# Performance work log

Measured on AMD Instinct MI355X. Metric: run time of the kernel, lower is better.

## Reference

```python
import jax, jax.numpy as jnp
import numpy as np
from jax import lax

K = 3  # deformable kernel size


def conv2d(x, w, b):
    # x: [B,C,H,W], w: [O,I,kh,kw], 'SAME' padding, stride 1
    out = lax.conv_general_dilated(x, w, (1, 1), 'SAME',
                                   dimension_numbers=('NCHW', 'OIHW', 'NCHW'))
    return out + b[None, :, None, None]


def deform_conv2d(x, dy, dx, mask, dw, db):
    # Deformable conv v2 (torchvision semantics): bilinear sample at
    # p0 + p_k + delta_p_k, zero outside, modulated by sigmoid mask.
    # x:[B,C,H,W]  dy,dx,mask:[B,H,W,K2]  dw:[O,C,K,K]  db:[O]
    B, C, H, W = x.shape
    K2 = K * K
    pad = K // 2
    ky = (jnp.arange(K2) // K).astype(x.dtype) - pad  # kernel row offsets
    kx = (jnp.arange(K2) % K).astype(x.dtype) - pad
    hy = jnp.arange(H, dtype=x.dtype)[:, None, None]
    wx = jnp.arange(W, dtype=x.dtype)[None, :, None]
    py = hy + ky[None, None, :] + dy  # [B,H,W,K2] sample rows
    px = wx + kx[None, None, :] + dx  # [B,H,W,K2] sample cols

    xf = x.reshape(B, C, H * W)
    gat = jax.vmap(lambda xfb, idx: xfb[:, idx])  # -> [B,C,H,W,K2]

    y0 = jnp.floor(py)
    x0 = jnp.floor(px)
    samp = jnp.zeros((B, C, H, W, K2), x.dtype)
    # accumulate the 4 bilinear corners (zero padding outside image)
    for yc, wy in ((y0, y0 + 1.0 - py), (y0 + 1.0, py - y0)):
        for xc, wxx in ((x0, x0 + 1.0 - px), (x0 + 1.0, px - x0)):
            valid = (yc >= 0) & (yc < H) & (xc >= 0) & (xc < W)
            idx = (jnp.clip(yc, 0, H - 1) * W
                   + jnp.clip(xc, 0, W - 1)).astype(jnp.int32)
            wgt = jnp.where(valid, wy * wxx, jnp.zeros((), x.dtype))
            samp = samp + gat(xf, idx) * wgt[:, None]  # [B,C,H,W,K2]

    samp = samp * mask[:, None]  # modulation: [B,1,H,W,K2]
    out = jnp.einsum('bchwk,ock->bohw', samp, dw.reshape(dw.shape[0], C, K2))
    return out + db[None, :, None, None]


def setup_inputs() -> dict:
    key = jax.random.key(0)
    ks = jax.random.split(key, 8)
    B, C, H, W = 8, 64, 128, 128
    K2 = K * K
    x = jax.random.normal(ks[0], (B, C, H, W), jnp.float32)
    # offset conv (3x3) -> 2*K2 channels; small init so offsets are modest
    ow = 0.02 * jax.random.normal(ks[1], (2 * K2, C, 3, 3), jnp.float32)
    ob = jnp.zeros((2 * K2,), jnp.float32)
    # mask conv (3x3) -> K2 channels
    mw = 0.02 * jax.random.normal(ks[2], (K2, C, 3, 3), jnp.float32)
    mb = jnp.zeros((K2,), jnp.float32)
    # deformable conv weights (C->C, KxK)
    dw = (1.0 / np.sqrt(C * K2)) * jax.random.normal(ks[3], (C, C, K, K), jnp.float32)
    db = jnp.zeros((C,), jnp.float32)
    return {'x': x, 'ow': ow, 'ob': ob, 'mw': mw, 'mb': mb, 'dw': dw, 'db': db}


def reference(x, ow, ob, mw, mb, dw, db):
    B, C, H, W = x.shape
    K2 = K * K
    offset = conv2d(x, ow, ob)                    # [B,2K2,H,W]
    mask = jax.nn.sigmoid(conv2d(x, mw, mb))      # [B,K2,H,W]
    off = offset.reshape(B, K2, 2, H, W)
    dy = off[:, :, 0].transpose(0, 2, 3, 1)       # [B,H,W,K2] (torchvision: even=dy)
    dx = off[:, :, 1].transpose(0, 2, 3, 1)
    return deform_conv2d(x, dy, dx, mask.transpose(0, 2, 3, 1), dw, db)
```

## Files before the change

### kernel.cpp

```cpp
#include <hip/hip_runtime.h>

#define BATCH 8
#define CIN   64
#define HW    16384
#define CK    576

typedef __attribute__((ext_vector_type(8))) short bf16x8;
typedef __attribute__((ext_vector_type(4))) float f32x4;
typedef __attribute__((ext_vector_type(2))) float f32x2;
typedef __attribute__((ext_vector_type(4))) unsigned u32x4;

__device__ inline unsigned short f2bf(float f) {
    unsigned int u = __builtin_bit_cast(unsigned int, f);
    u += 0x7FFFu + ((u >> 16) & 1u);
    return (unsigned short)(u >> 16);
}
__device__ inline float bf2f(unsigned short u) {
    return __builtin_bit_cast(float, (unsigned)u << 16);
}
__device__ inline f32x2 upk2(unsigned u) {
    f32x2 r;
    r[0] = __builtin_bit_cast(float, u << 16);
    r[1] = __builtin_bit_cast(float, u & 0xFFFF0000u);
    return r;
}
__device__ inline unsigned pk2bf(f32x2 s) {
    return (unsigned)f2bf(s[0]) | ((unsigned)f2bf(s[1]) << 16);
}


__global__ __launch_bounds__(256) void prep_transpose(
        const float* __restrict__ x, const float* __restrict__ ow,
        const float* __restrict__ mw, const float* __restrict__ dw,
        unsigned short* __restrict__ wpack, unsigned short* __restrict__ wcpack,
        unsigned short* __restrict__ xT) {
    __shared__ unsigned tile[64 * 36];
    int t = threadIdx.x, blk = blockIdx.x;
    int b = blk & 7, r2 = blk >> 3;
    int h = r2 >> 1, hf = r2 & 1;
    int px0 = hf << 6;
    {
        const float* __restrict__ xb = x + (b * CIN) * HW + (h << 7) + px0;
#pragma unroll
        for (int r = 0; r < 2; r++) {
            int g = r * 256 + t;
            int c2  = g >> 4;
            int col = (g & 15) << 2;
            f32x4 lo = *(const f32x4*)(xb + (2 * c2) * HW + col);
            f32x4 hi = *(const f32x4*)(xb + (2 * c2 + 1) * HW + col);
#pragma unroll
            for (int i = 0; i < 4; i++) {
                f32x2 s; s[0] = lo[i]; s[1] = hi[i];
                tile[(col + i) * 36 + c2] = pk2bf(s);
            }
        }
    }
    __syncthreads();
    {
        int p = t >> 2, q = t & 3;
        const unsigned* s = &tile[p * 36 + (q << 3)];
        u32x4 v0 = *(const u32x4*)(s);
        u32x4 v1 = *(const u32x4*)(s + 4);
        int pix = (h << 7) + px0 + p;
        unsigned short* dst = xT + ((b * HW + pix) << 6) + (q << 4);
        *(u32x4*)dst = v0;
        *(u32x4*)(dst + 8) = v1;
    }
    int g = blk * 256 + t;
    if (g < 18 * 4 * 64 * 8) {
        int j = g & 7, lane = (g >> 3) & 63, ot = (g >> 9) & 3, gks = g >> 11;
        int o = ot * 16 + (lane & 15);
        int s = gks * 32 + ((lane >> 4) & 3) * 8 + j;
        int c = s & 63, tap = s >> 6;
        wpack[g] = f2bf(dw[o * CK + c * 9 + tap]);
    }
    if (g < 18 * 2 * 64 * 8) {
        int j = g & 7, lane = (g >> 3) & 63, ot = (g >> 9) & 1, gks = g >> 10;
        int o = ot * 16 + (lane & 15);
        int s = gks * 32 + ((lane >> 4) & 3) * 8 + j;
        int c = s & 63, tap = s >> 6;
        float v = 0.f;
        if (o < 18)      v = ow[(o * 64 + c) * 9 + tap];
        else if (o < 27) v = mw[((o - 18) * 64 + c) * 9 + tap];
        wcpack[g] = f2bf(v);
    }
}

__global__ __launch_bounds__(256, 3) void fused_kernel(
        const unsigned short* __restrict__ xT, const unsigned short* __restrict__ wcpack,
        const unsigned short* __restrict__ wpack,
        const float* __restrict__ ob, const float* __restrict__ mb,
        const float* __restrict__ dbv, float* __restrict__ out) {
    __shared__ unsigned short buf[18560];
    __shared__ unsigned short omrow[2048];
    __shared__ int ptab[576];
    __shared__ float wtab[2304];

    int t = threadIdx.x;
    int lane = t & 63, pt = t >> 6, quad = lane >> 4, n = lane & 15;
    int blk = blockIdx.x;
    int b = blk & 7, r2 = blk >> 3;
    int h = r2 >> 1, hf = r2 & 1;
    int px0 = hf << 6;
    int pxl = (pt << 4) + n;
    int gx  = px0 + pxl;

    const unsigned short* __restrict__ xtb = xT + ((b * HW) << 6);
    const short zs = 0;
    const bf16x8 zv = {zs, zs, zs, zs, zs, zs, zs, zs};

    for (int i = t; i < 1584; i += 256) {
        int s  = i & 7;
        int rc = i >> 3;
        int r  = rc / 66, col = rc - r * 66;
        int gy  = h - 1 + r;
        int gxc = px0 - 1 + col;
        bf16x8 v = zv;
        if ((unsigned)gy < 128u && (unsigned)gxc < 128u)
            v = *(const bf16x8*)(xtb + (((gy << 7) + gxc) << 6) + (s << 3));
        *(bf16x8*)&buf[rc * 72 + (s << 3)] = v;
    }
    __syncthreads();

    {
        f32x4 acc0 = {0.f, 0.f, 0.f, 0.f}, acc1 = {0.f, 0.f, 0.f, 0.f};
#pragma unroll
        for (int tap = 0; tap < 9; tap++) {
            int r = tap / 3, cm = tap % 3;
            const unsigned short* srcA = &buf[(r * 66 + pxl + cm) * 72];
#pragma unroll
            for (int kk = 0; kk < 2; kk++) {
                bf16x8 bfrag = *(const bf16x8*)(srcA + (kk << 5) + (quad << 3));
                int gks = tap * 2 + kk;
                bf16x8 a0 = *(const bf16x8*)(wcpack + ((gks * 2 + 0) * 64 + lane) * 8);
                bf16x8 a1 = *(const bf16x8*)(wcpack + ((gks * 2 + 1) * 64 + lane) * 8);
                acc0 = __builtin_amdgcn_mfma_f32_16x16x32_bf16(a0, bfrag, acc0, 0, 0, 0);
                acc1 = __builtin_amdgcn_mfma_f32_16x16x32_bf16(a1, bfrag, acc1, 0, 0, 0);
            }
        }
        {
            unsigned short p[4];
#pragma unroll
            for (int r = 0; r < 4; r++) p[r] = f2bf(acc0[r] + ob[quad * 4 + r]);
            uint2 u;
            u.x = (unsigned)p[0] | ((unsigned)p[1] << 16);
            u.y = (unsigned)p[2] | ((unsigned)p[3] << 16);
            *(uint2*)&omrow[pxl * 32 + quad * 4] = u;
        }
        {
            unsigned short p[4];
#pragma unroll
            for (int r = 0; r < 4; r++) {
                int o = 16 + quad * 4 + r;
                float v = acc1[r];
                if (o < 18) v += ob[o];
                else if (o < 27) { v += mb[o - 18]; v = 1.f / (1.f + __expf(-v)); }
                else v = 0.f;
                p[r] = f2bf(v);
            }
            uint2 u;
            u.x = (unsigned)p[0] | ((unsigned)p[1] << 16);
            u.y = (unsigned)p[2] | ((unsigned)p[3] << 16);
            *(uint2*)&omrow[pxl * 32 + 16 + quad * 4] = u;
        }
    }
    __syncthreads();

#pragma unroll
    for (int k = 0; k < 9; k++) {
        float dy = bf2f(omrow[pxl * 32 + 2 * k]);
        float dx = bf2f(omrow[pxl * 32 + 2 * k + 1]);
        float mk = bf2f(omrow[pxl * 32 + 18 + k]);
        float py  = (float)h  + (float)(k / 3 - 1) + dy;
        float pxx = (float)gx + (float)(k % 3 - 1) + dx;
        float fy = floorf(py), fx = floorf(pxx);
        float ly = py - fy, lx = pxx - fx;
        int y0 = (int)fy, x0 = (int)fx;
        bool y0v = (unsigned)y0 < 128u, y1v = (unsigned)(y0 + 1) < 128u;
        bool x0v = (unsigned)x0 < 128u, x1v = (unsigned)(x0 + 1) < 128u;
        f32x4 wv;
        wv[0] = (y0v && x0v) ? (1.f - ly) * (1.f - lx) * mk : 0.f;
        wv[1] = (y0v && x1v) ? (1.f - ly) * lx * mk : 0.f;
        wv[2] = (y1v && x0v) ? ly * (1.f - lx) * mk : 0.f;
        wv[3] = (y1v && x1v) ? ly * lx * mk : 0.f;
        int y0c = min(max(y0, 0), 127), x0c = min(max(x0, 0), 127);
        int dxb = (x0 >= 0 && x0 < 127) ? 1 : 0;
        int dyb = (y0 >= 0 && y0 < 127) ? 1 : 0;
        if (quad == 0) {
            ptab[pxl * 9 + k] = ((y0c << 7) + x0c) | (dxb << 14) | (dyb << 15);
            *(f32x4*)&wtab[(pxl * 9 + k) * 4] = wv;
        }
    }
    __syncthreads();

    f32x4 acc[4];
#pragma unroll
    for (int ot = 0; ot < 4; ot++) acc[ot] = (f32x4){0.f, 0.f, 0.f, 0.f};

    unsigned short* gbw = &buf[(pt << 2) * 1160];
    int soff   = (lane & 7) << 3;
    int c2     = (lane >> 3) & 3;
    int cm1    = -(c2 & 1);
    int cm2    = -((c2 >> 1) & 1);
    int pxnb   = lane >> 5;
    int pibase = (pt << 4) * 9;
    int gwbase = c2 * 1160 + soff;
    int setbase = pxl * 9;

    bf16x8 pf[8];
#pragma unroll
    for (int i = 0; i < 8; i++) {
        int p = ptab[pibase + (pxnb + 2 * i) * 9];
        int row = (p & 0x3FFF) + (cm1 & ((p >> 14) & 1)) + (cm2 & (((p >> 15) & 1) << 7));
        pf[i] = *(const bf16x8*)(xtb + (row << 6) + soff);
    }

#pragma unroll
    for (int tap = 0; tap < 9; tap++) {
        bf16x8 nf[8];
        if (tap < 8) {
#pragma unroll
            for (int i = 0; i < 8; i++) {
                int p = ptab[pibase + (pxnb + 2 * i) * 9 + tap + 1];
                int row = (p & 0x3FFF) + (cm1 & ((p >> 14) & 1)) + (cm2 & (((p >> 15) & 1) << 7));
                nf[i] = *(const bf16x8*)(xtb + (row << 6) + soff);
            }
        }
#pragma unroll
        for (int i = 0; i < 8; i++)
            *(bf16x8*)&gbw[gwbase + (pxnb + 2 * i) * 72] = pf[i];

        f32x4 wv = *(const f32x4*)&wtab[(setbase + tap) * 4];
        f32x2 W0 = {wv[0], wv[0]}, W1 = {wv[1], wv[1]};
        f32x2 W2 = {wv[2], wv[2]}, W3 = {wv[3], wv[3]};
        const unsigned short* gbr = &gbw[n * 72];
#pragma unroll
        for (int kk = 0; kk < 2; kk++) {
            int co = (kk << 5) + (quad << 3);
            bf16x8 v00 = *(const bf16x8*)(gbr + 0 * 1160 + co);
            bf16x8 v01 = *(const bf16x8*)(gbr + 1 * 1160 + co);
            bf16x8 v10 = *(const bf16x8*)(gbr + 2 * 1160 + co);
            bf16x8 v11 = *(const bf16x8*)(gbr + 3 * 1160 + co);
            const unsigned* u00 = (const unsigned*)&v00;
            const unsigned* u01 = (const unsigned*)&v01;
            const unsigned* u10 = (const unsigned*)&v10;
            const unsigned* u11 = (const unsigned*)&v11;
            bf16x8 bfrag;
            unsigned* bu = (unsigned*)&bfrag;
#pragma unroll
            for (int jj = 0; jj < 4; jj++) {
                f32x2 s2 = upk2(u00[jj]) * W0 + upk2(u01[jj]) * W1
                         + upk2(u10[jj]) * W2 + upk2(u11[jj]) * W3;
                bu[jj] = pk2bf(s2);
            }
            int gks = tap * 2 + kk;
#pragma unroll
            for (int ot = 0; ot < 4; ot++) {
                bf16x8 af = *(const bf16x8*)(wpack + ((gks * 4 + ot) * 64 + lane) * 8);
                acc[ot] = __builtin_amdgcn_mfma_f32_16x16x32_bf16(af, bfrag, acc[ot], 0, 0, 0);
            }
        }
        if (tap < 8) {
#pragma unroll
            for (int i = 0; i < 8; i++) pf[i] = nf[i];
        }
    }

    int opix = (h << 7) + px0 + (pt << 4) + n;
#pragma unroll
    for (int ot = 0; ot < 4; ot++) {
#pragma unroll
        for (int r = 0; r < 4; r++) {
            int o = ot * 16 + quad * 4 + r;
            out[(b * 64 + o) * HW + opix] = acc[ot][r] + dbv[o];
        }
    }
}

extern "C" void kernel_launch(void* const* d_in, const int* in_sizes, int n_in,
                              void* d_out, int out_size, void* d_ws, size_t ws_size,
                              hipStream_t stream) {
    const float* x   = (const float*)d_in[0];
    const float* ow  = (const float*)d_in[1];
    const float* ob  = (const float*)d_in[2];
    const float* mw  = (const float*)d_in[3];
    const float* mb  = (const float*)d_in[4];
    const float* dw  = (const float*)d_in[5];
    const float* dbv = (const float*)d_in[6];
    float* out = (float*)d_out;

    unsigned short* wpack  = (unsigned short*)d_ws;
    unsigned short* wcpack = wpack + 36864;
    unsigned short* xT     = wpack + 55296;

    prep_transpose<<<2048, 256, 0, stream>>>(x, ow, mw, dw, wpack, wcpack, xT);
    fused_kernel<<<2048, 256, 0, stream>>>(xT, wcpack, wpack, ob, mb, dbv, out);
}
```

Measured before the change: 155.8 us.

## Gather bilinear corners directly into registers, dropping LDS staging and tables

Each lane now computes its own sampling rows and bilinear weights per tap and loads the four corner vectors straight from global memory into registers. This removes the ptab/wtab tables, the LDS staging buffer writes and reads, and one block barrier. The omrow layout becomes channel-major, and bf16 packing uses the hardware v_cvt_pk_bf16_f32 instruction. The smaller LDS footprint allows occupancy to rise to 4 blocks per CU. In exchange, every quad lane redundantly recomputes the sampling parameters, and the gathers are now scattered per lane rather than coalesced per row.

Result: slower. 185.2 us (+18.9%).

```diff
diff --git a/kernel.cpp b/kernel.cpp
--- a/kernel.cpp
+++ b/kernel.cpp
@@ -26,6 +26,11 @@
 }
 __device__ inline unsigned pk2bf(f32x2 s) {
     return (unsigned)f2bf(s[0]) | ((unsigned)f2bf(s[1]) << 16);
+}
+__device__ inline unsigned cvtpk(float lo, float hi) {
+    unsigned r;
+    asm("v_cvt_pk_bf16_f32 %0, %1, %2" : "=v"(r) : "v"(lo), "v"(hi));
+    return r;
 }
 
 
@@ -86,15 +91,13 @@
     }
 }
 
-__global__ __launch_bounds__(256, 3) void fused_kernel(
+__global__ __launch_bounds__(256, 4) void fused_kernel(
         const unsigned short* __restrict__ xT, const unsigned short* __restrict__ wcpack,
         const unsigned short* __restrict__ wpack,
         const float* __restrict__ ob, const float* __restrict__ mb,
         const float* __restrict__ dbv, float* __restrict__ out) {
-    __shared__ unsigned short buf[18560];
+    __shared__ unsigned short buf[14256];
     __shared__ unsigned short omrow[2048];
-    __shared__ int ptab[576];
-    __shared__ float wtab[2304];
 
     int t = threadIdx.x;
     int lane = t & 63, pt = t >> 6, quad = lane >> 4, n = lane & 15;
@@ -138,39 +141,33 @@
                 acc1 = __builtin_amdgcn_mfma_f32_16x16x32_bf16(a1, bfrag, acc1, 0, 0, 0);
             }
         }
-        {
-            unsigned short p[4];
-#pragma unroll
-            for (int r = 0; r < 4; r++) p[r] = f2bf(acc0[r] + ob[quad * 4 + r]);
-            uint2 u;
-            u.x = (unsigned)p[0] | ((unsigned)p[1] << 16);
-            u.y = (unsigned)p[2] | ((unsigned)p[3] << 16);
-            *(uint2*)&omrow[pxl * 32 + quad * 4] = u;
-        }
-        {
-            unsigned short p[4];
-#pragma unroll
-            for (int r = 0; r < 4; r++) {
-                int o = 16 + quad * 4 + r;
-                float v = acc1[r];
-                if (o < 18) v += ob[o];
-                else if (o < 27) { v += mb[o - 18]; v = 1.f / (1.f + __expf(-v)); }
-                else v = 0.f;
-                p[r] = f2bf(v);
-            }
-            uint2 u;
-            u.x = (unsigned)p[0] | ((unsigned)p[1] << 16);
-            u.y = (unsigned)p[2] | ((unsigned)p[3] << 16);
-            *(uint2*)&omrow[pxl * 32 + 16 + quad * 4] = u;
+#pragma unroll
+        for (int r = 0; r < 4; r++) {
+            int o = quad * 4 + r;
+            omrow[o * 64 + pxl] = f2bf(acc0[r] + ob[o]);
+        }
+#pragma unroll
+        for (int r = 0; r < 4; r++) {
+            int o = 16 + quad * 4 + r;
+            float v = acc1[r];
+            if (o < 18) v += ob[o];
+            else if (o < 27) { v += mb[o - 18]; v = 1.f / (1.f + __expf(-v)); }
+            else v = 0.f;
+            omrow[o * 64 + pxl] = f2bf(v);
         }
     }
     __syncthreads();
 
-#pragma unroll
-    for (int k = 0; k < 9; k++) {
-        float dy = bf2f(omrow[pxl * 32 + 2 * k]);
-        float dx = bf2f(omrow[pxl * 32 + 2 * k + 1]);
-        float mk = bf2f(omrow[pxl * 32 + 18 + k]);
+    f32x4 acc[4];
+#pragma unroll
+    for (int ot = 0; ot < 4; ot++) acc[ot] = (f32x4){0.f, 0.f, 0.f, 0.f};
+
+    int coff = quad << 3;
+
+    auto params = [&](int k, int* rows, f32x4& wv) {
+        float dy = bf2f(omrow[(2 * k) * 64 + pxl]);
+        float dx = bf2f(omrow[(2 * k + 1) * 64 + pxl]);
+        float mk = bf2f(omrow[(18 + k) * 64 + pxl]);
         float py  = (float)h  + (float)(k / 3 - 1) + dy;
         float pxx = (float)gx + (float)(k % 3 - 1) + dx;
         float fy = floorf(py), fx = floorf(pxx);
@@ -178,80 +175,54 @@
         int y0 = (int)fy, x0 = (int)fx;
         bool y0v = (unsigned)y0 < 128u, y1v = (unsigned)(y0 + 1) < 128u;
         bool x0v = (unsigned)x0 < 128u, x1v = (unsigned)(x0 + 1) < 128u;
-        f32x4 wv;
         wv[0] = (y0v && x0v) ? (1.f - ly) * (1.f - lx) * mk : 0.f;
         wv[1] = (y0v && x1v) ? (1.f - ly) * lx * mk : 0.f;
         wv[2] = (y1v && x0v) ? ly * (1.f - lx) * mk : 0.f;
         wv[3] = (y1v && x1v) ? ly * lx * mk : 0.f;
         int y0c = min(max(y0, 0), 127), x0c = min(max(x0, 0), 127);
         int dxb = (x0 >= 0 && x0 < 127) ? 1 : 0;
-        int dyb = (y0 >= 0 && y0 < 127) ? 1 : 0;
-        if (quad == 0) {
-            ptab[pxl * 9 + k] = ((y0c << 7) + x0c) | (dxb << 14) | (dyb << 15);
-            *(f32x4*)&wtab[(pxl * 9 + k) * 4] = wv;
-        }
-    }
-    __syncthreads();
-
-    f32x4 acc[4];
-#pragma unroll
-    for (int ot = 0; ot < 4; ot++) acc[ot] = (f32x4){0.f, 0.f, 0.f, 0.f};
-
-    unsigned short* gbw = &buf[(pt << 2) * 1160];
-    int soff   = (lane & 7) << 3;
-    int c2     = (lane >> 3) & 3;
-    int cm1    = -(c2 & 1);
-    int cm2    = -((c2 >> 1) & 1);
-    int pxnb   = lane >> 5;
-    int pibase = (pt << 4) * 9;
-    int gwbase = c2 * 1160 + soff;
-    int setbase = pxl * 9;
-
+        int dyb = (y0 >= 0 && y0 < 127) ? (1 << 7) : 0;
+        int r00 = (y0c << 7) + x0c;
+        rows[0] = r00; rows[1] = r00 + dxb;
+        rows[2] = r00 + dyb; rows[3] = r00 + dyb + dxb;
+    };
+
+    int rows0[4]; f32x4 wcur;
+    params(0, rows0, wcur);
     bf16x8 pf[8];
 #pragma unroll
-    for (int i = 0; i < 8; i++) {
-        int p = ptab[pibase + (pxnb + 2 * i) * 9];
-        int row = (p & 0x3FFF) + (cm1 & ((p >> 14) & 1)) + (cm2 & (((p >> 15) & 1) << 7));
-        pf[i] = *(const bf16x8*)(xtb + (row << 6) + soff);
-    }
+    for (int c = 0; c < 4; c++)
+#pragma unroll
+        for (int kk = 0; kk < 2; kk++)
+            pf[c * 2 + kk] = *(const bf16x8*)(xtb + (rows0[c] << 6) + (kk << 5) + coff);
 
 #pragma unroll
     for (int tap = 0; tap < 9; tap++) {
-        bf16x8 nf[8];
+        bf16x8 nf[8]; f32x4 wnext;
         if (tap < 8) {
-#pragma unroll
-            for (int i = 0; i < 8; i++) {
-                int p = ptab[pibase + (pxnb + 2 * i) * 9 + tap + 1];
-                int row = (p & 0x3FFF) + (cm1 & ((p >> 14) & 1)) + (cm2 & (((p >> 15) & 1) << 7));
-                nf[i] = *(const bf16x8*)(xtb + (row << 6) + soff);
-            }
-        }
-#pragma unroll
-        for (int i = 0; i < 8; i++)
-            *(bf16x8*)&gbw[gwbase + (pxnb + 2 * i) * 72] = pf[i];
-
-        f32x4 wv = *(const f32x4*)&wtab[(setbase + tap) * 4];
-        f32x2 W0 = {wv[0], wv[0]}, W1 = {wv[1], wv[1]};
-        f32x2 W2 = {wv[2], wv[2]}, W3 = {wv[3], wv[3]};
-        const unsigned short* gbr = &gbw[n * 72];
+            int nrows[4];
+            params(tap + 1, nrows, wnext);
+#pragma unroll
+            for (int c = 0; c < 4; c++)
+#pragma unroll
+                for (int kk = 0; kk < 2; kk++)
+                    nf[c * 2 + kk] = *(const bf16x8*)(xtb + (nrows[c] << 6) + (kk << 5) + coff);
+        }
+        f32x2 W0 = {wcur[0], wcur[0]}, W1 = {wcur[1], wcur[1]};
+        f32x2 W2 = {wcur[2], wcur[2]}, W3 = {wcur[3], wcur[3]};
 #pragma unroll
         for (int kk = 0; kk < 2; kk++) {
-            int co = (kk << 5) + (quad << 3);
-            bf16x8 v00 = *(const bf16x8*)(gbr + 0 * 1160 + co);
-            bf16x8 v01 = *(const bf16x8*)(gbr + 1 * 1160 + co);
-            bf16x8 v10 = *(const bf16x8*)(gbr + 2 * 1160 + co);
-            bf16x8 v11 = *(const bf16x8*)(gbr + 3 * 1160 + co);
-            const unsigned* u00 = (const unsigned*)&v00;
-            const unsigned* u01 = (const unsigned*)&v01;
-            const unsigned* u10 = (const unsigned*)&v10;
-            const unsigned* u11 = (const unsigned*)&v11;
+            const unsigned* u00 = (const unsigned*)&pf[0 * 2 + kk];
+            const unsigned* u01 = (const unsigned*)&pf[1 * 2 + kk];
+            const unsigned* u10 = (const unsigned*)&pf[2 * 2 + kk];
+            const unsigned* u11 = (const unsigned*)&pf[3 * 2 + kk];
             bf16x8 bfrag;
             unsigned* bu = (unsigned*)&bfrag;
 #pragma unroll
             for (int jj = 0; jj < 4; jj++) {
                 f32x2 s2 = upk2(u00[jj]) * W0 + upk2(u01[jj]) * W1
                          + upk2(u10[jj]) * W2 + upk2(u11[jj]) * W3;
-                bu[jj] = pk2bf(s2);
+                bu[jj] = cvtpk(s2[0], s2[1]);
             }
             int gks = tap * 2 + kk;
 #pragma unroll
@@ -263,6 +234,7 @@
         if (tap < 8) {
 #pragma unroll
             for (int i = 0; i < 8; i++) pf[i] = nf[i];
+            wcur = wnext;
         }
     }
 
```
